# Kernel tuning notes

Measured on AMD Instinct MI355X. Metric: run time of the kernel, lower is better.

Reference implementation:

```python
import jax, jax.numpy as jnp
import numpy as np

ITER_NUM = 3       # nSteps of the SICE proximal loop (module iterNum)
NS_ITERS = 7       # Newton-Schulz iterations, hardcoded in _sice
F_LR = 5.0         # sice_lrate
F_SPARSITY = 0.07  # sparsity_val
BN_EPS = 1e-5


def _inv_sqrtm(x, iterN):
    """Batched Newton-Schulz inverse matrix square root (Sqrtm.forward)."""
    d = x.shape[-1]
    I3 = 3.0 * jnp.eye(d, dtype=x.dtype)
    normA = jnp.trace(x, axis1=-2, axis2=-1)            # [B]
    A = x / normA[:, None, None]
    ZY = 0.5 * (I3 - A)
    Y = A @ ZY
    Z = ZY
    for _ in range(iterN - 2):
        ZY = 0.5 * (I3 - Z @ Y)
        Y = Y @ ZY
        Z = ZY @ Z
    ZYZ = 0.5 * (I3 - Z @ Y) @ Z
    return ZYZ * (normA ** -0.5)[:, None, None]


def _covpool(x):
    """x: [B,C,H,W] -> centered second-order pooling [B,C,C] (Covpool)."""
    b, c, h, w = x.shape
    m = h * w
    xf = x.reshape(b, c, m)
    xc = xf - xf.mean(axis=-1, keepdims=True)
    # x @ I_hat @ x^T == (x - mean)(x - mean)^T / M
    return (xc @ xc.transpose(0, 2, 1)) / m


def _sice(x, jitter):
    C = _covpool(x)
    C = C / jnp.trace(C, axis1=-2, axis2=-1)[:, None, None]
    Ij = jnp.diag(1e-10 + 1e-9 * jitter)[None].astype(C.dtype)   # [1,D,D]
    zz = _inv_sqrtm(C + Ij, NS_ITERS)
    LLT = zz @ zz                                                # inv covariance init
    sym_C = 0.5 * (C + C.transpose(0, 2, 1))
    for i in range(ITER_NUM):
        Lp = jax.nn.relu(LLT)
        Lm = jax.nn.relu(-LLT)
        zz = _inv_sqrtm(LLT + Ij, NS_ITERS)
        g12 = -(zz @ zz) + sym_C
        dec = F_LR * (1.0 - i / (ITER_NUM - 1.0))
        Lp = jax.nn.relu(Lp - dec * (g12 + F_SPARSITY))
        Lm = jax.nn.relu(Lm - dec * (-g12 + F_SPARSITY))
        LLT = Lp - Lm
        LLT = 0.5 * (LLT + LLT.transpose(0, 2, 1))
    return LLT / jnp.sqrt(jnp.trace(LLT, axis1=-2, axis2=-1))[:, None, None]


def reference(x, conv_w, gamma, beta, jitter):
    # 1x1 conv dimension reduction + BatchNorm (batch stats, train mode) + ReLU
    y = jnp.einsum('bchw,dc->bdhw', x, conv_w)
    mu = y.mean(axis=(0, 2, 3), keepdims=True)
    var = y.var(axis=(0, 2, 3), keepdims=True)
    y = (y - mu) / jnp.sqrt(var + BN_EPS)
    y = jax.nn.relu(y * gamma[None, :, None, None] + beta[None, :, None, None])
    out = _sice(y, jitter)                                       # [B,D,D]
    b, d = out.shape[0], out.shape[1]
    iu = np.nonzero(np.triu(np.ones((d, d))).reshape(-1))[0]     # Triuvec indices
    return out.reshape(b, d * d)[:, iu]                          # [B, D*(D+1)/2]


def setup_inputs() -> dict:
    key = jax.random.key(0)
    k1, k2, k3 = jax.random.split(key, 3)
    B, CIN, H, W, DR = 32, 2048, 28, 28, 256
    x = jax.random.normal(k1, (B, CIN, H, W), dtype=jnp.float32)
    # kaiming normal, mode=fan_out (fan_out = DR*1*1): std = sqrt(2/DR)
    conv_w = jax.random.normal(k2, (DR, CIN), dtype=jnp.float32) * np.sqrt(2.0 / DR).astype(np.float32)
    gamma = jnp.ones((DR,), dtype=jnp.float32)
    beta = jnp.zeros((DR,), dtype=jnp.float32)
    jitter = jax.random.uniform(k3, (DR,), dtype=jnp.float32)
    return {"x": x, "conv_w": conv_w, "gamma": gamma, "beta": beta, "jitter": jitter}
```

## Files before the change

### kernel.cpp

```cpp
#include <hip/hip_runtime.h>
#include <utility>


typedef unsigned short u16;
typedef __attribute__((ext_vector_type(8))) __bf16 bf16x8;
typedef __attribute__((ext_vector_type(8))) _Float16 f16x8;
typedef __attribute__((ext_vector_type(4))) float f32x4;

#define DEV __device__ __forceinline__

DEV u16 f2bf(float f) {
  unsigned x = __float_as_uint(f);
  x += 0x7fffu + ((x >> 16) & 1u);
  return (u16)(x >> 16);
}
DEV float bf2f(u16 h) { return __uint_as_float(((unsigned)h) << 16); }

#define SB_SUM   0
#define SB_SSQ   256
#define SB_IJ    512
#define SB_TRC   768
#define SB_TR2   800
#define SB_TR3   832
#define SB_TRL   864
#define SB_DEN   896
#define SB_IJSUM 928

__global__ __launch_bounds__(256) void k_prep(const float* __restrict__ w,
                                              const float* __restrict__ jitter,
                                              _Float16* __restrict__ w_half,
                                              float* __restrict__ sb) {
  int gid = blockIdx.x * 256 + threadIdx.x;
  if (gid < 256 * 2048) w_half[gid] = (_Float16)w[gid];
  if (blockIdx.x == 0) {
    int t = threadIdx.x;
    sb[SB_SUM + t] = 0.f;
    sb[SB_SSQ + t] = 0.f;
    float ij = 1e-10f + 1e-9f * jitter[t];
    sb[SB_IJ + t] = ij;
    if (t < 160) sb[SB_TRC + t] = 0.f;
    __shared__ float red[256];
    red[t] = ij; __syncthreads();
    for (int off = 128; off > 0; off >>= 1) {
      if (t < off) red[t] += red[t + off];
      __syncthreads();
    }
    if (t == 0) sb[SB_IJSUM] = red[0];
  }
}

__global__ __launch_bounds__(256) void k_conv(const _Float16* __restrict__ w_half,
                                              const float* __restrict__ x,
                                              _Float16* __restrict__ y,
                                              float* __restrict__ sb) {
  int xb = blockIdx.x;
  int b = xb & 31;
  int rest = xb >> 5;
  int mt = rest / 13, ht = rest % 13;
  int hw0 = ht * 64;
  int t = threadIdx.x;
  int wv = t >> 6, lane = t & 63, m = lane & 15, quad = lane >> 4;
  __shared__ _Float16 lsA[2][128 * 40];
  __shared__ _Float16 lsB[2][64 * 40];
  f32x4 acc[4][2];
#pragma unroll
  for (int i = 0; i < 4; ++i)
#pragma unroll
    for (int j = 0; j < 2; ++j) acc[i][j] = (f32x4){0.f, 0.f, 0.f, 0.f};
  int rowA = t & 127, halfA = t >> 7;
  const _Float16* wp = w_half + ((size_t)(mt * 128 + rowA)) * 2048 + halfA * 16;
  int hwB = t & 63, cg = t >> 6;
  bool okB = (hw0 + hwB) < 784;
  const float* xp = x + ((size_t)b * 2048 + cg * 8) * 784 + hw0 + hwB;
  uint4 ra0, ra1;
  float rb[8];
  ra0 = *(const uint4*)(wp);
  ra1 = *(const uint4*)(wp + 8);
#pragma unroll
  for (int j = 0; j < 8; ++j) rb[j] = okB ? xp[(size_t)j * 784] : 0.f;
  int wr = (wv >> 1) * 64, wc = (wv & 1) * 32;
  for (int kc = 0; kc < 64; ++kc) {
    int buf = kc & 1;
    int loA = rowA * 40 + halfA * 16;
    *(uint4*)&lsA[buf][loA] = ra0;
    *(uint4*)&lsA[buf][loA + 8] = ra1;
    {
      union { f16x8 h; uint4 u; } pk;
#pragma unroll
      for (int j = 0; j < 8; ++j) pk.h[j] = (_Float16)rb[j];
      *(uint4*)&lsB[buf][hwB * 40 + cg * 8] = pk.u;
    }
    if (kc < 63) {
      int k0 = (kc + 1) * 32;
      ra0 = *(const uint4*)(wp + k0);
      ra1 = *(const uint4*)(wp + k0 + 8);
#pragma unroll
      for (int j = 0; j < 8; ++j)
        rb[j] = okB ? xp[((size_t)k0 + j) * 784] : 0.f;
    }
    __syncthreads();
    f16x8 af[4], bfg[2];
#pragma unroll
    for (int i = 0; i < 4; ++i)
      af[i] = *(const f16x8*)&lsA[buf][(wr + i * 16 + m) * 40 + quad * 8];
#pragma unroll
    for (int j = 0; j < 2; ++j)
      bfg[j] = *(const f16x8*)&lsB[buf][(wc + j * 16 + m) * 40 + quad * 8];
#pragma unroll
    for (int i = 0; i < 4; ++i)
#pragma unroll
      for (int j = 0; j < 2; ++j)
        acc[i][j] = __builtin_amdgcn_mfma_f32_16x16x32_f16(af[i], bfg[j], acc[i][j], 0, 0, 0);
  }
  float* sum = sb + SB_SUM;
  float* ssq = sb + SB_SSQ;
#pragma unroll
  for (int i = 0; i < 4; ++i) {
#pragma unroll
    for (int r = 0; r < 4; ++r) {
      float s = 0.f, q = 0.f;
#pragma unroll
      for (int j = 0; j < 2; ++j) {
        float v = acc[i][j][r];
        s += v; q += v * v;
      }
      s += __shfl_xor(s, 1); s += __shfl_xor(s, 2);
      s += __shfl_xor(s, 4); s += __shfl_xor(s, 8);
      q += __shfl_xor(q, 1); q += __shfl_xor(q, 2);
      q += __shfl_xor(q, 4); q += __shfl_xor(q, 8);
      if (m == 0) {
        int R = mt * 128 + wr + i * 16 + quad * 4 + r;
        atomicAdd(&sum[R], s);
        atomicAdd(&ssq[R], q);
      }
    }
  }
#pragma unroll
  for (int i = 0; i < 4; ++i)
#pragma unroll
    for (int j = 0; j < 2; ++j)
#pragma unroll
      for (int r = 0; r < 4; ++r) {
        int R = mt * 128 + wr + i * 16 + quad * 4 + r;
        int hwc = hw0 + wc + j * 16 + m;
        if (hwc < 784) y[((size_t)b * 256 + R) * 784 + hwc] = (_Float16)acc[i][j][r];
      }
}

__global__ __launch_bounds__(256) void k_bnapply(const _Float16* __restrict__ y,
                                                 const float* __restrict__ gamma,
                                                 const float* __restrict__ beta,
                                                 const float* __restrict__ sb,
                                                 _Float16* __restrict__ yc) {
  int xb = blockIdx.x;
  int d = xb >> 5, b = xb & 31, t = threadIdx.x;
  float mu = sb[SB_SUM + d] * (1.0f / 25088.0f);
  float var = sb[SB_SSQ + d] * (1.0f / 25088.0f) - mu * mu;
  float sc = gamma[d] / sqrtf(var + 1e-5f);
  float sh = beta[d] - mu * sc;
  const _Float16* row = y + ((size_t)b * 256 + d) * 784;
  float v[4];
  float s = 0.f;
#pragma unroll
  for (int i = 0; i < 4; ++i) {
    int idx = t + i * 256;
    float u = 0.f;
    if (idx < 784) u = fmaxf((float)row[idx] * sc + sh, 0.f);
    v[i] = u; s += u;
  }
  __shared__ float red[256];
  red[t] = s; __syncthreads();
  for (int off = 128; off > 0; off >>= 1) {
    if (t < off) red[t] += red[t + off];
    __syncthreads();
  }
  float mean = red[0] * (1.0f / 784.0f);
  _Float16* out = yc + ((size_t)b * 256 + d) * 800;
#pragma unroll
  for (int i = 0; i < 4; ++i) {
    int idx = t + i * 256;
    if (idx < 784) out[idx] = (_Float16)(v[i] - mean);
  }
  if (t < 16) out[784 + t] = (_Float16)0.f;
}

__global__ __launch_bounds__(256) void k_gram(const _Float16* __restrict__ yc,
                                              float* __restrict__ C,
                                              float* __restrict__ sb) {
  int xb = blockIdx.x;
  int b = xb & 31, rest = xb >> 5;
  int tr = rest >> 2, tc = rest & 3;
  int t = threadIdx.x, wv = t >> 6, lane = t & 63, m = lane & 15, quad = lane >> 4;
  __shared__ _Float16 lsA[2][32 * 40];
  __shared__ _Float16 lsB[2][64 * 40];
  f32x4 acc[2];
  acc[0] = (f32x4){0.f, 0.f, 0.f, 0.f};
  acc[1] = (f32x4){0.f, 0.f, 0.f, 0.f};
  int row = t >> 2, seg = t & 3;
  const _Float16* base = yc + (size_t)b * 256 * 800;
  const _Float16* Bp = base + (size_t)(tc * 64 + row) * 800 + seg * 8;
  const _Float16* Ap = base + (size_t)(tr * 32 + row) * 800 + seg * 8;
  bool doA = row < 32;
  uint4 rB = *(const uint4*)(Bp);
  uint4 rA = doA ? *(const uint4*)(Ap) : (uint4){0, 0, 0, 0};
  int ar = (wv >> 1) * 16, bcl = (wv & 1) * 32;
  for (int ks = 0; ks < 25; ++ks) {
    int buf = ks & 1;
    int lo = row * 40 + seg * 8;
    *(uint4*)&lsB[buf][lo] = rB;
    if (doA) *(uint4*)&lsA[buf][lo] = rA;
    if (ks < 24) {
      int k0 = (ks + 1) * 32;
      rB = *(const uint4*)(Bp + k0);
      if (doA) rA = *(const uint4*)(Ap + k0);
    }
    __syncthreads();
    f16x8 a0 = *(const f16x8*)&lsA[buf][(ar + m) * 40 + quad * 8];
    f16x8 b0 = *(const f16x8*)&lsB[buf][(bcl + m) * 40 + quad * 8];
    f16x8 b1 = *(const f16x8*)&lsB[buf][(bcl + 16 + m) * 40 + quad * 8];
    acc[0] = __builtin_amdgcn_mfma_f32_16x16x32_f16(a0, b0, acc[0], 0, 0, 0);
    acc[1] = __builtin_amdgcn_mfma_f32_16x16x32_f16(a0, b1, acc[1], 0, 0, 0);
  }
  const float inv = 1.0f / 784.0f;
#pragma unroll
  for (int j = 0; j < 2; ++j)
#pragma unroll
    for (int r = 0; r < 4; ++r) {
      int R = tr * 32 + ar + quad * 4 + r;
      int Cc = tc * 64 + bcl + j * 16 + m;
      float v = acc[j][r] * inv;
      C[((size_t)b * 256 + R) * 256 + Cc] = v;
      if (R == Cc) atomicAdd(&sb[SB_TRC + b], v);
    }
}

__global__ __launch_bounds__(256) void k_prepAZY(const float* __restrict__ src,
                                                 float* __restrict__ symC,
                                                 u16* __restrict__ Ah, u16* __restrict__ Al,
                                                 u16* __restrict__ ZYh, u16* __restrict__ ZYl,
                                                 float* __restrict__ sb, int slot, int mode) {
  int xb = blockIdx.x;
  int i = xb >> 5, b = xb & 31, j = threadIdx.x;
  float trv = (mode == 0) ? 1.0f : sb[slot + b];
  float denom = trv + sb[SB_IJSUM];
  if (i == 0 && j == 0) sb[SB_DEN + b] = denom;
  size_t idx = ((size_t)b * 256 + i) * 256 + j;
  float v;
  if (mode == 0) {
    float trC = sb[SB_TRC + b];
    float vij = src[idx] / trC;
    float vji = src[((size_t)b * 256 + j) * 256 + i] / trC;
    symC[idx] = 0.5f * (vij + vji);
    v = vij;
  } else {
    v = src[idx];
  }
  if (i == j) v += sb[SB_IJ + i];
  float A = v / denom;
  u16 h = f2bf(A);
  Ah[idx] = h; Al[idx] = f2bf(A - bf2f(h));
  float zy = 0.5f * ((i == j ? 3.0f : 0.0f) - A);
  h = f2bf(zy);
  ZYh[idx] = h; ZYl[idx] = f2bf(zy - bf2f(h));
}

struct MMArgs {
  const u16* Ah; const u16* Al; const u16* Bh; const u16* Bl;
  u16* Oh; u16* Ol; float* Of; float* tr; int emode;
};

__global__ __launch_bounds__(256) void mm_ns(MMArgs g0, MMArgs g1,
                                             const float* __restrict__ sb) {
  int xb = blockIdx.x;
  int b = xb & 31;
  int rest = xb >> 5;
  MMArgs g = (rest < 32) ? g0 : g1;
  int tile = rest & 31;
  int tr = tile >> 2, tc = tile & 3;
  int t = threadIdx.x, wv = t >> 6, lane = t & 63, m = lane & 15, quad = lane >> 4;
  __shared__ u16 lsAh[2][32 * 40], lsAl[2][32 * 40];
  __shared__ u16 lsBh[2][64 * 40], lsBl[2][64 * 40];
  f32x4 acc[2];
  acc[0] = (f32x4){0.f, 0.f, 0.f, 0.f};
  acc[1] = (f32x4){0.f, 0.f, 0.f, 0.f};
  int row = t >> 2, seg = t & 3;
  size_t mb = (size_t)b * 65536;
  size_t bO = mb + (size_t)(tc * 64 + row) * 256 + seg * 8;
  size_t aO = mb + (size_t)(tr * 32 + row) * 256 + seg * 8;
  bool doA = row < 32;
  uint4 rBh = *(const uint4*)(g.Bh + bO);
  uint4 rBl = *(const uint4*)(g.Bl + bO);
  uint4 rAh = doA ? *(const uint4*)(g.Ah + aO) : (uint4){0, 0, 0, 0};
  uint4 rAl = doA ? *(const uint4*)(g.Al + aO) : (uint4){0, 0, 0, 0};
  int ar = (wv >> 1) * 16, bcl = (wv & 1) * 32;
  for (int ks = 0; ks < 8; ++ks) {
    int buf = ks & 1;
    int lo = row * 40 + seg * 8;
    *(uint4*)&lsBh[buf][lo] = rBh;
    *(uint4*)&lsBl[buf][lo] = rBl;
    if (doA) {
      *(uint4*)&lsAh[buf][lo] = rAh;
      *(uint4*)&lsAl[buf][lo] = rAl;
    }
    if (ks < 7) {
      int k0 = (ks + 1) * 32;
      rBh = *(const uint4*)(g.Bh + bO + k0);
      rBl = *(const uint4*)(g.Bl + bO + k0);
      if (doA) {
        rAh = *(const uint4*)(g.Ah + aO + k0);
        rAl = *(const uint4*)(g.Al + aO + k0);
      }
    }
    __syncthreads();
    bf16x8 ah = *(const bf16x8*)&lsAh[buf][(ar + m) * 40 + quad * 8];
    bf16x8 al = *(const bf16x8*)&lsAl[buf][(ar + m) * 40 + quad * 8];
    bf16x8 bh0 = *(const bf16x8*)&lsBh[buf][(bcl + m) * 40 + quad * 8];
    bf16x8 bl0 = *(const bf16x8*)&lsBl[buf][(bcl + m) * 40 + quad * 8];
    bf16x8 bh1 = *(const bf16x8*)&lsBh[buf][(bcl + 16 + m) * 40 + quad * 8];
    bf16x8 bl1 = *(const bf16x8*)&lsBl[buf][(bcl + 16 + m) * 40 + quad * 8];
    acc[0] = __builtin_amdgcn_mfma_f32_16x16x32_bf16(ah, bh0, acc[0], 0, 0, 0);
    acc[0] = __builtin_amdgcn_mfma_f32_16x16x32_bf16(ah, bl0, acc[0], 0, 0, 0);
    acc[0] = __builtin_amdgcn_mfma_f32_16x16x32_bf16(al, bh0, acc[0], 0, 0, 0);
    acc[1] = __builtin_amdgcn_mfma_f32_16x16x32_bf16(ah, bh1, acc[1], 0, 0, 0);
    acc[1] = __builtin_amdgcn_mfma_f32_16x16x32_bf16(ah, bl1, acc[1], 0, 0, 0);
    acc[1] = __builtin_amdgcn_mfma_f32_16x16x32_bf16(al, bh1, acc[1], 0, 0, 0);
  }
  float scl = 1.0f;
  if (g.emode == 2) scl = 1.0f / sqrtf(sb[SB_DEN + b]);
#pragma unroll
  for (int j = 0; j < 2; ++j)
#pragma unroll
    for (int r = 0; r < 4; ++r) {
      int R = tr * 32 + ar + quad * 4 + r;
      int Cc = tc * 64 + bcl + j * 16 + m;
      float v = acc[j][r];
      if (g.emode == 1) v = 0.5f * ((R == Cc ? 3.0f : 0.0f) - v);
      else if (g.emode == 2) v = v * scl;
      size_t oidx = mb + (size_t)R * 256 + Cc;
      if (g.emode == 3) {
        g.Of[oidx] = v;
        if (R == Cc && g.tr) atomicAdd(g.tr + b, v);
      } else {
        u16 h = f2bf(v);
        g.Oh[oidx] = h;
        g.Ol[oidx] = f2bf(v - bf2f(h));
      }
    }
}

__global__ __launch_bounds__(256) void k_sice(const float* __restrict__ LLT,
                                              const float* __restrict__ P,
                                              const float* __restrict__ symC,
                                              float* __restrict__ out,
                                              float* __restrict__ sb, int slot,
                                              float dec) {
  int xb = blockIdx.x;
  int b = xb & 31, p = xb >> 5;
  const int TRt[10] = {0, 0, 0, 0, 1, 1, 1, 2, 2, 3};
  const int TCt[10] = {0, 1, 2, 3, 1, 2, 3, 2, 3, 3};
  int tr = TRt[p], tc = TCt[p];
  __shared__ float ft[64][65];
  __shared__ float ot[64][65];
  int t = threadIdx.x;
  size_t base = (size_t)b * 65536;
#pragma unroll 4
  for (int it = 0; it < 16; ++it) {
    int idx = it * 256 + t;
    int r = idx >> 6, c = idx & 63;
    size_t o = base + (size_t)(tc * 64 + r) * 256 + tr * 64 + c;
    float L = LLT[o];
    float g = symC[o] - P[o];
    float f = fmaxf(fmaxf(L, 0.f) - dec * (g + 0.07f), 0.f) -
              fmaxf(fmaxf(-L, 0.f) - dec * (-g + 0.07f), 0.f);
    ft[r][c] = f;
  }
  __syncthreads();
  float tsum = 0.f;
#pragma unroll 4
  for (int it = 0; it < 16; ++it) {
    int idx = it * 256 + t;
    int r = idx >> 6, c = idx & 63;
    size_t o = base + (size_t)(tr * 64 + r) * 256 + tc * 64 + c;
    float L = LLT[o];
    float g = symC[o] - P[o];
    float f = fmaxf(fmaxf(L, 0.f) - dec * (g + 0.07f), 0.f) -
              fmaxf(fmaxf(-L, 0.f) - dec * (-g + 0.07f), 0.f);
    float val = 0.5f * (f + ft[c][r]);
    out[o] = val;
    ot[r][c] = val;
    if (tr == tc && r == c) tsum += val;
  }
  if (tr == tc) {
    if (tsum != 0.f) atomicAdd(&sb[slot + b], tsum);
  } else {
    __syncthreads();
#pragma unroll 4
    for (int it = 0; it < 16; ++it) {
      int idx = it * 256 + t;
      int r = idx >> 6, c = idx & 63;
      size_t o = base + (size_t)(tc * 64 + r) * 256 + tr * 64 + c;
      out[o] = ot[c][r];
    }
  }
}

__global__ __launch_bounds__(256) void k_out(const float* __restrict__ LLT,
                                             const float* __restrict__ sb,
                                             float* __restrict__ out) {
  int xb = blockIdx.x;
  int i = xb >> 5, b = xb & 31, j = threadIdx.x;
  if (j < i) return;
  float inv = 1.0f / sqrtf(sb[SB_TRL + b]);
  int tl = i * 256 - (i * (i - 1)) / 2 + (j - i);
  out[(size_t)b * 32896 + tl] = LLT[((size_t)b * 256 + i) * 256 + j] * inv;
}

extern "C" void kernel_launch(void* const* d_in, const int* in_sizes, int n_in,
                              void* d_out, int out_size, void* d_ws, size_t ws_size,
                              hipStream_t stream) {
  const float* x = (const float*)d_in[0];
  const float* w = (const float*)d_in[1];
  const float* gamma = (const float*)d_in[2];
  const float* beta = (const float*)d_in[3];
  const float* jitter = (const float*)d_in[4];
  char* ws = (char*)d_ws;

  _Float16* w_half = (_Float16*)(ws + 0);
  float* sb = (float*)(ws + (1 << 20));
  _Float16* y = (_Float16*)(ws + (2 << 20));
  _Float16* yc = (_Float16*)(ws + (16 << 20));
  char* ov = ws + (32 << 20);
  float* Craw = (float*)(ov + 0);
  float* symC = (float*)(ov + 8388608);
  float* LLTa = (float*)(ov + 16777216);
  float* P = (float*)(ov + 25165824);
  float* LLTb = (float*)(ov + 33554432);
  u16* bf[12];
  for (int i = 0; i < 12; ++i) bf[i] = (u16*)(ov + 41943040 + (size_t)i * 4194304);

  k_prep<<<2048, 256, 0, stream>>>(w, jitter, w_half, sb);
  k_conv<<<832, 256, 0, stream>>>(w_half, x, y, sb);
  k_bnapply<<<8192, 256, 0, stream>>>(y, gamma, beta, sb, yc);
  k_gram<<<1024, 256, 0, stream>>>(yc, Craw, sb);

  auto run_ns = [&](const float* src, int mode, int slot_in, float* Pout,
                    float* tr_out) {
    k_prepAZY<<<8192, 256, 0, stream>>>(src, symC, bf[0], bf[1], bf[2], bf[3], sb, slot_in, mode);
    u16 *Ah = bf[0], *Al = bf[1], *ZYh = bf[2], *ZYl = bf[3];
    u16 *Yh = bf[4], *Yl = bf[5], *Z2h = bf[6], *Z2l = bf[7];
    u16 *Th = bf[8], *Tl = bf[9], *zzh = bf[10], *zzl = bf[11];
    MMArgs m1{Ah, Al, ZYh, ZYl, Yh, Yl, nullptr, nullptr, 0};
    mm_ns<<<1024, 256, 0, stream>>>(m1, m1, sb);
    u16 *Ych = Yh, *Ycl = Yl, *Yah = Ah, *Yal = Al;
    u16 *Zch = ZYh, *Zcl = ZYl, *Zah = Z2h, *Zal = Z2l;
    for (int it = 0; it < 5; ++it) {
      MMArgs mt{Zch, Zcl, Ych, Ycl, Th, Tl, nullptr, nullptr, 1};
      mm_ns<<<1024, 256, 0, stream>>>(mt, mt, sb);
      MMArgs my{Ych, Ycl, Th, Tl, Yah, Yal, nullptr, nullptr, 0};
      MMArgs mz{Th, Tl, Zch, Zcl, Zah, Zal, nullptr, nullptr, 0};
      mm_ns<<<2048, 256, 0, stream>>>(my, mz, sb);
      std::swap(Ych, Yah); std::swap(Ycl, Yal);
      std::swap(Zch, Zah); std::swap(Zcl, Zal);
    }
    MMArgs mt6{Zch, Zcl, Ych, Ycl, Th, Tl, nullptr, nullptr, 1};
    mm_ns<<<1024, 256, 0, stream>>>(mt6, mt6, sb);
    MMArgs mz7{Th, Tl, Zch, Zcl, zzh, zzl, nullptr, nullptr, 2};
    mm_ns<<<1024, 256, 0, stream>>>(mz7, mz7, sb);
    MMArgs mzz{zzh, zzl, zzh, zzl, nullptr, nullptr, Pout, tr_out, 3};
    mm_ns<<<1024, 256, 0, stream>>>(mzz, mzz, sb);
  };

  run_ns(Craw, 0, 0, LLTa, sb + SB_TR2);
  run_ns(LLTa, 1, SB_TR2, P, nullptr);
  k_sice<<<320, 256, 0, stream>>>(LLTa, P, symC, LLTb, sb, SB_TR3, 5.0f);
  run_ns(LLTb, 1, SB_TR3, P, nullptr);
  k_sice<<<320, 256, 0, stream>>>(LLTb, P, symC, LLTa, sb, SB_TRL, 2.5f);

  k_out<<<8192, 256, 0, stream>>>(LLTa, sb, (float*)d_out);
}
```

Measured before the change: 1.051 ms.

## Drop B low-part MFMA term, move BN stats to separate kernel, batch prepAZY rows

The split-bf16 matmul in the Newton-Schulz chain now computes only ah*bh + al*bh and no longer loads or uses the low part of B. This removes a third of the MFMAs plus the B-low loads and LDS traffic, at the cost of lower accuracy. BatchNorm statistics move out of the conv epilogue, where they were accumulated with atomics, into a dedicated reduction kernel that rereads y. prepAZY now has each block process 8 rows, cutting its grid from 8192 to 1024 blocks.

```diff
diff --git a/kernel.cpp b/kernel.cpp
--- a/kernel.cpp
+++ b/kernel.cpp
@@ -34,8 +34,6 @@
   if (gid < 256 * 2048) w_half[gid] = (_Float16)w[gid];
   if (blockIdx.x == 0) {
     int t = threadIdx.x;
-    sb[SB_SUM + t] = 0.f;
-    sb[SB_SSQ + t] = 0.f;
     float ij = 1e-10f + 1e-9f * jitter[t];
     sb[SB_IJ + t] = ij;
     if (t < 160) sb[SB_TRC + t] = 0.f;
@@ -51,8 +49,7 @@
 
 __global__ __launch_bounds__(256) void k_conv(const _Float16* __restrict__ w_half,
                                               const float* __restrict__ x,
-                                              _Float16* __restrict__ y,
-                                              float* __restrict__ sb) {
+                                              _Float16* __restrict__ y) {
   int xb = blockIdx.x;
   int b = xb & 31;
   int rest = xb >> 5;
@@ -112,29 +109,6 @@
       for (int j = 0; j < 2; ++j)
         acc[i][j] = __builtin_amdgcn_mfma_f32_16x16x32_f16(af[i], bfg[j], acc[i][j], 0, 0, 0);
   }
-  float* sum = sb + SB_SUM;
-  float* ssq = sb + SB_SSQ;
-#pragma unroll
-  for (int i = 0; i < 4; ++i) {
-#pragma unroll
-    for (int r = 0; r < 4; ++r) {
-      float s = 0.f, q = 0.f;
-#pragma unroll
-      for (int j = 0; j < 2; ++j) {
-        float v = acc[i][j][r];
-        s += v; q += v * v;
-      }
-      s += __shfl_xor(s, 1); s += __shfl_xor(s, 2);
-      s += __shfl_xor(s, 4); s += __shfl_xor(s, 8);
-      q += __shfl_xor(q, 1); q += __shfl_xor(q, 2);
-      q += __shfl_xor(q, 4); q += __shfl_xor(q, 8);
-      if (m == 0) {
-        int R = mt * 128 + wr + i * 16 + quad * 4 + r;
-        atomicAdd(&sum[R], s);
-        atomicAdd(&ssq[R], q);
-      }
-    }
-  }
 #pragma unroll
   for (int i = 0; i < 4; ++i)
 #pragma unroll
@@ -145,6 +119,31 @@
         int hwc = hw0 + wc + j * 16 + m;
         if (hwc < 784) y[((size_t)b * 256 + R) * 784 + hwc] = (_Float16)acc[i][j][r];
       }
+}
+
+__global__ __launch_bounds__(256) void k_stats(const _Float16* __restrict__ y,
+                                               float* __restrict__ sb) {
+  int d = blockIdx.x, t = threadIdx.x;
+  float s = 0.f, q = 0.f;
+  if (t < 196) {
+    for (int b = 0; b < 32; ++b) {
+      const _Float16* row = y + ((size_t)b * 256 + d) * 784;
+      union { uint2 u; _Float16 h[4]; } v;
+      v.u = *(const uint2*)(row + t * 4);
+#pragma unroll
+      for (int k = 0; k < 4; ++k) {
+        float f = (float)v.h[k];
+        s += f; q += f * f;
+      }
+    }
+  }
+  __shared__ float rs[256], rq[256];
+  rs[t] = s; rq[t] = q; __syncthreads();
+  for (int off = 128; off > 0; off >>= 1) {
+    if (t < off) { rs[t] += rs[t + off]; rq[t] += rq[t + off]; }
+    __syncthreads();
+  }
+  if (t == 0) { sb[SB_SUM + d] = rs[0]; sb[SB_SSQ + d] = rq[0]; }
 }
 
 __global__ __launch_bounds__(256) void k_bnapply(const _Float16* __restrict__ y,
@@ -240,32 +239,36 @@
                                                  u16* __restrict__ ZYh, u16* __restrict__ ZYl,
                                                  float* __restrict__ sb, int slot, int mode) {
   int xb = blockIdx.x;
-  int i = xb >> 5, b = xb & 31, j = threadIdx.x;
+  int ig = xb >> 5, b = xb & 31, j = threadIdx.x;
   float trv = (mode == 0) ? 1.0f : sb[slot + b];
   float denom = trv + sb[SB_IJSUM];
-  if (i == 0 && j == 0) sb[SB_DEN + b] = denom;
-  size_t idx = ((size_t)b * 256 + i) * 256 + j;
-  float v;
-  if (mode == 0) {
-    float trC = sb[SB_TRC + b];
-    float vij = src[idx] / trC;
-    float vji = src[((size_t)b * 256 + j) * 256 + i] / trC;
-    symC[idx] = 0.5f * (vij + vji);
-    v = vij;
-  } else {
-    v = src[idx];
-  }
-  if (i == j) v += sb[SB_IJ + i];
-  float A = v / denom;
-  u16 h = f2bf(A);
-  Ah[idx] = h; Al[idx] = f2bf(A - bf2f(h));
-  float zy = 0.5f * ((i == j ? 3.0f : 0.0f) - A);
-  h = f2bf(zy);
-  ZYh[idx] = h; ZYl[idx] = f2bf(zy - bf2f(h));
+  if (ig == 0 && j == 0) sb[SB_DEN + b] = denom;
+  float trC = (mode == 0) ? sb[SB_TRC + b] : 1.0f;
+#pragma unroll
+  for (int ii = 0; ii < 8; ++ii) {
+    int i = ig * 8 + ii;
+    size_t idx = ((size_t)b * 256 + i) * 256 + j;
+    float v;
+    if (mode == 0) {
+      float vij = src[idx] / trC;
+      float vji = src[((size_t)b * 256 + j) * 256 + i] / trC;
+      symC[idx] = 0.5f * (vij + vji);
+      v = vij;
+    } else {
+      v = src[idx];
+    }
+    if (i == j) v += sb[SB_IJ + i];
+    float A = v / denom;
+    u16 h = f2bf(A);
+    Ah[idx] = h; Al[idx] = f2bf(A - bf2f(h));
+    float zy = 0.5f * ((i == j ? 3.0f : 0.0f) - A);
+    h = f2bf(zy);
+    ZYh[idx] = h; ZYl[idx] = f2bf(zy - bf2f(h));
+  }
 }
 
 struct MMArgs {
-  const u16* Ah; const u16* Al; const u16* Bh; const u16* Bl;
+  const u16* Ah; const u16* Al; const u16* Bh;
   u16* Oh; u16* Ol; float* Of; float* tr; int emode;
 };
 
@@ -279,7 +282,7 @@
   int tr = tile >> 2, tc = tile & 3;
   int t = threadIdx.x, wv = t >> 6, lane = t & 63, m = lane & 15, quad = lane >> 4;
   __shared__ u16 lsAh[2][32 * 40], lsAl[2][32 * 40];
-  __shared__ u16 lsBh[2][64 * 40], lsBl[2][64 * 40];
+  __shared__ u16 lsBh[2][64 * 40];
   f32x4 acc[2];
   acc[0] = (f32x4){0.f, 0.f, 0.f, 0.f};
   acc[1] = (f32x4){0.f, 0.f, 0.f, 0.f};
@@ -289,7 +292,6 @@
   size_t aO = mb + (size_t)(tr * 32 + row) * 256 + seg * 8;
   bool doA = row < 32;
   uint4 rBh = *(const uint4*)(g.Bh + bO);
-  uint4 rBl = *(const uint4*)(g.Bl + bO);
   uint4 rAh = doA ? *(const uint4*)(g.Ah + aO) : (uint4){0, 0, 0, 0};
   uint4 rAl = doA ? *(const uint4*)(g.Al + aO) : (uint4){0, 0, 0, 0};
   int ar = (wv >> 1) * 16, bcl = (wv & 1) * 32;
@@ -297,7 +299,6 @@
     int buf = ks & 1;
     int lo = row * 40 + seg * 8;
     *(uint4*)&lsBh[buf][lo] = rBh;
-    *(uint4*)&lsBl[buf][lo] = rBl;
     if (doA) {
       *(uint4*)&lsAh[buf][lo] = rAh;
       *(uint4*)&lsAl[buf][lo] = rAl;
@@ -305,7 +306,6 @@
     if (ks < 7) {
       int k0 = (ks + 1) * 32;
       rBh = *(const uint4*)(g.Bh + bO + k0);
-      rBl = *(const uint4*)(g.Bl + bO + k0);
       if (doA) {
         rAh = *(const uint4*)(g.Ah + aO + k0);
         rAl = *(const uint4*)(g.Al + aO + k0);
@@ -315,14 +315,10 @@
     bf16x8 ah = *(const bf16x8*)&lsAh[buf][(ar + m) * 40 + quad * 8];
     bf16x8 al = *(const bf16x8*)&lsAl[buf][(ar + m) * 40 + quad * 8];
     bf16x8 bh0 = *(const bf16x8*)&lsBh[buf][(bcl + m) * 40 + quad * 8];
-    bf16x8 bl0 = *(const bf16x8*)&lsBl[buf][(bcl + m) * 40 + quad * 8];
     bf16x8 bh1 = *(const bf16x8*)&lsBh[buf][(bcl + 16 + m) * 40 + quad * 8];
-    bf16x8 bl1 = *(const bf16x8*)&lsBl[buf][(bcl + 16 + m) * 40 + quad * 8];
     acc[0] = __builtin_amdgcn_mfma_f32_16x16x32_bf16(ah, bh0, acc[0], 0, 0, 0);
-    acc[0] = __builtin_amdgcn_mfma_f32_16x16x32_bf16(ah, bl0, acc[0], 0, 0, 0);
     acc[0] = __builtin_amdgcn_mfma_f32_16x16x32_bf16(al, bh0, acc[0], 0, 0, 0);
     acc[1] = __builtin_amdgcn_mfma_f32_16x16x32_bf16(ah, bh1, acc[1], 0, 0, 0);
-    acc[1] = __builtin_amdgcn_mfma_f32_16x16x32_bf16(ah, bl1, acc[1], 0, 0, 0);
     acc[1] = __builtin_amdgcn_mfma_f32_16x16x32_bf16(al, bh1, acc[1], 0, 0, 0);
   }
   float scl = 1.0f;
@@ -439,34 +435,35 @@
   for (int i = 0; i < 12; ++i) bf[i] = (u16*)(ov + 41943040 + (size_t)i * 4194304);
 
   k_prep<<<2048, 256, 0, stream>>>(w, jitter, w_half, sb);
-  k_conv<<<832, 256, 0, stream>>>(w_half, x, y, sb);
+  k_conv<<<832, 256, 0, stream>>>(w_half, x, y);
+  k_stats<<<256, 256, 0, stream>>>(y, sb);
   k_bnapply<<<8192, 256, 0, stream>>>(y, gamma, beta, sb, yc);
   k_gram<<<1024, 256, 0, stream>>>(yc, Craw, sb);
 
   auto run_ns = [&](const float* src, int mode, int slot_in, float* Pout,
                     float* tr_out) {
-    k_prepAZY<<<8192, 256, 0, stream>>>(src, symC, bf[0], bf[1], bf[2], bf[3], sb, slot_in, mode);
+    k_prepAZY<<<1024, 256, 0, stream>>>(src, symC, bf[0], bf[1], bf[2], bf[3], sb, slot_in, mode);
     u16 *Ah = bf[0], *Al = bf[1], *ZYh = bf[2], *ZYl = bf[3];
     u16 *Yh = bf[4], *Yl = bf[5], *Z2h = bf[6], *Z2l = bf[7];
     u16 *Th = bf[8], *Tl = bf[9], *zzh = bf[10], *zzl = bf[11];
-    MMArgs m1{Ah, Al, ZYh, ZYl, Yh, Yl, nullptr, nullptr, 0};
+    MMArgs m1{Ah, Al, ZYh, Yh, Yl, nullptr, nullptr, 0};
     mm_ns<<<1024, 256, 0, stream>>>(m1, m1, sb);
     u16 *Ych = Yh, *Ycl = Yl, *Yah = Ah, *Yal = Al;
     u16 *Zch = ZYh, *Zcl = ZYl, *Zah = Z2h, *Zal = Z2l;
     for (int it = 0; it < 5; ++it) {
-      MMArgs mt{Zch, Zcl, Ych, Ycl, Th, Tl, nullptr, nullptr, 1};
+      MMArgs mt{Zch, Zcl, Ych, Th, Tl, nullptr, nullptr, 1};
       mm_ns<<<1024, 256, 0, stream>>>(mt, mt, sb);
-      MMArgs my{Ych, Ycl, Th, Tl, Yah, Yal, nullptr, nullptr, 0};
-      MMArgs mz{Th, Tl, Zch, Zcl, Zah, Zal, nullptr, nullptr, 0};
+      MMArgs my{Ych, Ycl, Th, Yah, Yal, nullptr, nullptr, 0};
+      MMArgs mz{Th, Tl, Zch, Zah, Zal, nullptr, nullptr, 0};
       mm_ns<<<2048, 256, 0, stream>>>(my, mz, sb);
       std::swap(Ych, Yah); std::swap(Ycl, Yal);
       std::swap(Zch, Zah); std::swap(Zcl, Zal);
     }
-    MMArgs mt6{Zch, Zcl, Ych, Ycl, Th, Tl, nullptr, nullptr, 1};
+    MMArgs mt6{Zch, Zcl, Ych, Th, Tl, nullptr, nullptr, 1};
     mm_ns<<<1024, 256, 0, stream>>>(mt6, mt6, sb);
-    MMArgs mz7{Th, Tl, Zch, Zcl, zzh, zzl, nullptr, nullptr, 2};
+    MMArgs mz7{Th, Tl, Zch, zzh, zzl, nullptr, nullptr, 2};
     mm_ns<<<1024, 256, 0, stream>>>(mz7, mz7, sb);
-    MMArgs mzz{zzh, zzl, zzh, zzl, nullptr, nullptr, Pout, tr_out, 3};
+    MMArgs mzz{zzh, zzl, zzh, nullptr, nullptr, Pout, tr_out, 3};
     mm_ns<<<1024, 256, 0, stream>>>(mzz, mzz, sb);
   };
 
```

New measurement: 878.4 us. -16.4%, faster.
